# Kernel tuning notes

Hardware: AMD Instinct MI355X
Metric: run time of the kernel (lower is better)

Reference implementation:

```python
import jax, jax.numpy as jnp
import numpy as np


def setup_inputs() -> dict:
    key = jax.random.key(0)
    pred = jax.random.normal(key, (16, 4, 768, 768), dtype=jnp.float32)
    return {"pred": pred}


def _largest_cc(mask):
    """Largest 4-connected component of a 2D boolean mask, as float32 0/1.

    Equivalent to scipy.ndimage.label (default 4-connectivity) followed by
    keeping the largest label. Uses min-label flood propagation: each
    foreground pixel starts with its raster index; iterated neighbor-min
    converges so every pixel holds its component's minimum pixel index
    (the 'root'). Ties in size resolve to the smallest root, which matches
    scipy's label-order tie-breaking (labels assigned in raster order).
    """
    H, W = mask.shape
    HW = H * W
    idx = jnp.arange(HW, dtype=jnp.int32).reshape(H, W)
    BIG = jnp.int32(HW)  # sentinel for background
    lbl0 = jnp.where(mask, idx, BIG)

    def body(carry):
        lbl, _ = carry
        p = jnp.pad(lbl, 1, constant_values=HW)
        nb = jnp.minimum(jnp.minimum(p[:-2, 1:-1], p[2:, 1:-1]),
                         jnp.minimum(p[1:-1, :-2], p[1:-1, 2:]))
        new = jnp.where(mask, jnp.minimum(lbl, nb), BIG)
        return new, jnp.any(new != lbl)

    lbl, _ = jax.lax.while_loop(lambda c: c[1], body, (lbl0, jnp.any(mask)))

    # component sizes keyed by root pixel index; background bucket = HW
    sizes = jax.ops.segment_sum(mask.ravel().astype(jnp.int32), lbl.ravel(),
                                num_segments=HW + 1)
    sizes = sizes.at[HW].set(0)
    root = jnp.argmax(sizes).astype(jnp.int32)
    return ((lbl == root) & mask).astype(jnp.float32)


def reference(pred):
    B, C, H, W = pred.shape
    labels = jnp.argmax(pred, axis=1)  # [B, H, W]
    cls = jnp.arange(1, C, dtype=labels.dtype)
    masks = labels[:, None, :, :] == cls[None, :, None, None]  # [B, C-1, H, W]
    comp = jax.vmap(_largest_cc)(masks.reshape(-1, H, W)).reshape(B, C - 1, H, W)
    bg = 1.0 - jnp.clip(comp.sum(axis=1), 0.0, 1.0)  # channel 0
    return jnp.concatenate([bg[:, None], comp], axis=1)
```

## Files before the change

kernel.cpp:

```cpp
#include <hip/hip_runtime.h>
#include <stdint.h>

#define BB 16
#define CC 4
#define HH 768
#define WW 768
#define HW (HH * WW)
#define NPIX (BB * HW)
#define NIMG (BB * (CC - 1))
#define BEST_STRIDE 16

#define TS 64
#define TPI (WW / TS)
#define TILES_PER_IMG (TPI * TPI)
#define TPIX (TS * TS)
#define CCL_TPB 256

typedef unsigned long long ull;


__device__ __forceinline__ int find_root(int* P, int i) {
    int p = P[i];
    while (p != i) {
        int gp = P[p];
        P[i] = gp;
        i = p;
        p = gp;
    }
    return i;
}

__device__ __forceinline__ void merge(int* P, int a, int b) {
    a = find_root(P, a);
    b = find_root(P, b);
    while (a != b) {
        if (a < b) { int t = a; a = b; b = t; }
        int old = atomicCAS(&P[a], a, b);
        if (old == a) return;
        a = find_root(P, old);
        b = find_root(P, b);
    }
}


__device__ __forceinline__ int lfind(int* P, int i) {
    int p = P[i];
    while (p != i) {
        int gp = P[p];
        P[i] = gp;
        i = p;
        p = gp;
    }
    return i;
}

__device__ __forceinline__ void lmerge(int* P, int a, int b) {
    a = lfind(P, a);
    b = lfind(P, b);
    while (a != b) {
        if (a < b) { int t = a; a = b; b = t; }
        int old = atomicCAS(&P[a], a, b);
        if (old == a) return;
        a = lfind(P, old);
        b = lfind(P, b);
    }
}

__device__ __forceinline__ ull umax64(ull a, ull b) { return a > b ? a : b; }


__global__ __launch_bounds__(CCL_TPB) void k_tile_ccl(
        const float* __restrict__ pred,
        uint8_t* __restrict__ labels,
        int* __restrict__ parent,
        uint32_t* __restrict__ counts,
        ull* __restrict__ best) {
    __shared__ __align__(16) int sp[TPIX];
    __shared__ __align__(16) uint8_t slab[TPIX];
    __shared__ int changed;

    if (blockIdx.x == 0) {
        for (int i = threadIdx.x; i < NIMG * BEST_STRIDE; i += CCL_TPB) best[i] = 0ull;
    }

    const int tid = (int)threadIdx.x;
    const int img = blockIdx.x / TILES_PER_IMG;
    const int tile = blockIdx.x % TILES_PER_IMG;
    const int tr = (tile / TPI) * TS;
    const int tc = (tile % TPI) * TS;
    const float* pb = pred + (size_t)img * CC * HW;
    const int imgbase = img * HW;

    for (int k = 0; k < TPIX; k += CCL_TPB * 4) {
        int li = k + tid * 4;
        int gi = (tr + (li >> 6)) * WW + tc + (li & 63);
        float4 v0 = *(const float4*)&pb[gi];
        float4 v1 = *(const float4*)&pb[gi + HW];
        float4 v2 = *(const float4*)&pb[gi + 2 * HW];
        float4 v3 = *(const float4*)&pb[gi + 3 * HW];
        const float* a0 = &v0.x; const float* a1 = &v1.x;
        const float* a2 = &v2.x; const float* a3 = &v3.x;
        uchar4 lout;
        uint8_t* lj = &lout.x;
        #pragma unroll
        for (int j = 0; j < 4; ++j) {
            int lab = 0;
            float bv = a0[j];
            if (a1[j] > bv) { bv = a1[j]; lab = 1; }
            if (a2[j] > bv) { bv = a2[j]; lab = 2; }
            if (a3[j] > bv) { bv = a3[j]; lab = 3; }
            lj[j] = (uint8_t)lab;
        }
        *(uchar4*)&slab[li] = lout;
        *(uchar4*)&labels[imgbase + gi] = lout;
    }
    __syncthreads();

    const int c = tid & 63;

    #pragma unroll 1
    for (int it = 0; it < TPIX / CCL_TPB; ++it) {
        int li = it * CCL_TPB + tid;
        int lab = slab[li];
        int labL = __shfl_up(lab, 1, 64);
        bool isStart = lab && (c == 0 || labL != lab);
        ull mask = __ballot(isStart);
        int v = li;
        if (lab) {
            ull mle = mask & (~0ull >> (63 - c));
            v = (li & ~63) + (63 - __clzll(mle));
        }
        sp[li] = v;
    }
    __syncthreads();

    #pragma unroll 1
    for (int it = 0; it < TPIX / CCL_TPB; ++it) {
        int li = it * CCL_TPB + tid;
        int lab = slab[li];
        int labU = (li >= TS) ? (int)slab[li - TS] : 0;
        int labL = __shfl_up(lab, 1, 64);
        int labUL = __shfl_up(labU, 1, 64);
        if (lab && labU == lab) {
            if (c == 0 || !(labL == lab && labUL == lab))
                lmerge(sp, li, li - TS);
        }
    }
    __syncthreads();

    for (;;) {
        if (tid == 0) changed = 0;
        __syncthreads();
        int any = 0;
        #pragma unroll 1
        for (int it = 0; it < TPIX / CCL_TPB; ++it) {
            int li = it * CCL_TPB + tid;
            int v = sp[li];
            int w = sp[v];
            if (w != v) { sp[li] = w; any = 1; }
        }
        if (any) changed = 1;
        __syncthreads();
        int go = changed;
        __syncthreads();
        if (!go) break;
    }

    #pragma unroll 1
    for (int it = 0; it < TPIX / CCL_TPB; ++it) {
        int li = it * CCL_TPB + tid;
        int lab = slab[li];
        int labL = __shfl_up(lab, 1, 64);
        bool isStart = lab && (c == 0 || labL != lab);
        bool isEnd = lab && (c == 63 || (int)slab[li + 1] != lab);
        ull endmask = __ballot(isEnd);
        if (isStart) {
            ull mge = endmask & (~0ull << c);
            int epos = __ffsll((long long)mge) - 1;
            int runlen = epos - c + 1;
            int root = sp[li] & 0xFFFF;
            atomicAdd((unsigned int*)&sp[root], (unsigned int)runlen << 16);
        }
    }
    __syncthreads();

    for (int k = 0; k < TPIX; k += CCL_TPB * 4) {
        int li = k + tid * 4;
        int gi = imgbase + (tr + (li >> 6)) * WW + tc + (li & 63);
        uchar4 lv = *(const uchar4*)&slab[li];
        int4 sv = *(const int4*)&sp[li];
        const uint8_t* lj = &lv.x;
        const int* sj = &sv.x;
        int4 pout; uint4 cout;
        int* pj = &pout.x; uint32_t* cj = &cout.x;
        #pragma unroll
        for (int j = 0; j < 4; ++j) {
            int root = sj[j] & 0xFFFF;
            if (lj[j]) {
                pj[j] = imgbase + (tr + (root >> 6)) * WW + tc + (root & 63);
                cj[j] = (root == li + j) ? ((uint32_t)sj[j] >> 16) : 0u;
            } else {
                pj[j] = -1;
                cj[j] = 0u;
            }
        }
        *(int4*)&parent[gi] = pout;
        *(uint4*)&counts[gi] = cout;
    }
}

#define VEDGES ((TPI - 1) * HH)
#define EDGES_PER_IMG (2 * (TPI - 1) * HH)
__global__ void k_border_merge(const uint8_t* __restrict__ labels, int* parent) {
    int t = blockIdx.x * blockDim.x + threadIdx.x;
    if (t >= BB * EDGES_PER_IMG) return;
    int img = t / EDGES_PER_IMG;
    int e = t % EDGES_PER_IMG;
    int a, b;
    if (e < VEDGES) {
        int j = e / HH, r = e % HH;
        int c = j * TS + TS - 1;
        a = r * WW + c;
        b = a + 1;
    } else {
        e -= VEDGES;
        int j = e / WW, c = e % WW;
        int r = j * TS + TS - 1;
        a = r * WW + c;
        b = a + WW;
    }
    int ga = img * HW + a, gb = img * HW + b;
    uint8_t la = labels[ga];
    if (la && labels[gb] == la) merge(parent, ga, gb);
}

__global__ void k_compress(int* __restrict__ parent, uint32_t* __restrict__ counts) {
    int t = blockIdx.x * blockDim.x + threadIdx.x;
    if (t >= NPIX) return;
    uint32_t cnt = counts[t];
    if (!cnt) return;
    int g = parent[t];
    if (g == t) return;
    while (true) { int pg = parent[g]; if (pg == g) break; g = pg; }
    parent[t] = g;
    atomicAdd(&counts[g], cnt);
    counts[t] = 0;
}

#define BEST_BLK_PER_IMG 144
#define BEST_TPB 256
#define BEST_PIX_PER_BLK (HW / BEST_BLK_PER_IMG)
__global__ void k_best(const uint8_t* __restrict__ labels,
                       const uint32_t* __restrict__ counts,
                       ull* __restrict__ best) {
    __shared__ ull sw[(BEST_TPB / 64) * 3];
    int img = blockIdx.x / BEST_BLK_PER_IMG;
    int chunk = blockIdx.x % BEST_BLK_PER_IMG;
    int base = img * HW + chunk * BEST_PIX_PER_BLK;

    ull l0 = 0, l1 = 0, l2 = 0;
    for (int k = 0; k < BEST_PIX_PER_BLK; k += BEST_TPB * 4) {
        int t = base + k + (int)threadIdx.x * 4;
        uint4 cv = *(const uint4*)&counts[t];
        if (cv.x | cv.y | cv.z | cv.w) {
            uchar4 lv = *(const uchar4*)&labels[t];
            uint32_t cs[4] = {cv.x, cv.y, cv.z, cv.w};
            uint8_t ls[4] = {lv.x, lv.y, lv.z, lv.w};
            #pragma unroll
            for (int j = 0; j < 4; ++j) {
                if (cs[j]) {
                    int cc = (int)ls[j] - 1;
                    ull key = ((ull)cs[j] << 32) | (ull)(~(uint32_t)(t + j));
                    if (cc == 0) l0 = umax64(l0, key);
                    else if (cc == 1) l1 = umax64(l1, key);
                    else l2 = umax64(l2, key);
                }
            }
        }
    }
    #pragma unroll
    for (int m = 1; m < 64; m <<= 1) {
        l0 = umax64(l0, __shfl_xor(l0, m, 64));
        l1 = umax64(l1, __shfl_xor(l1, m, 64));
        l2 = umax64(l2, __shfl_xor(l2, m, 64));
    }
    int lane = threadIdx.x & 63;
    int wid = threadIdx.x >> 6;
    if (lane == 0) { sw[wid * 3 + 0] = l0; sw[wid * 3 + 1] = l1; sw[wid * 3 + 2] = l2; }
    __syncthreads();
    if (threadIdx.x < 3) {
        ull m = 0;
        for (int w = 0; w < BEST_TPB / 64; ++w) m = umax64(m, sw[w * 3 + threadIdx.x]);
        if (m) atomicMax(&best[(img * 3 + (int)threadIdx.x) * BEST_STRIDE], m);
    }
}

__global__ void k_output(const uint8_t* __restrict__ labels,
                         const int* __restrict__ parent,
                         const ull* __restrict__ best,
                         float* __restrict__ out) {
    int q = blockIdx.x * blockDim.x + threadIdx.x;
    if (q >= NPIX / 4) return;
    int t = q * 4;
    int b = t / HW;
    int i = t - b * HW;
    uchar4 lv = *(const uchar4*)&labels[t];
    int4 pv = *(const int4*)&parent[t];
    int root[3];
    root[0] = (int)(~(uint32_t)best[(b * 3 + 0) * BEST_STRIDE]);
    root[1] = (int)(~(uint32_t)best[(b * 3 + 1) * BEST_STRIDE]);
    root[2] = (int)(~(uint32_t)best[(b * 3 + 2) * BEST_STRIDE]);

    uint8_t ls[4] = {lv.x, lv.y, lv.z, lv.w};
    int ps[4] = {pv.x, pv.y, pv.z, pv.w};
    float fg[4];
    #pragma unroll
    for (int j = 0; j < 4; ++j) {
        int g = -1;
        if (ps[j] >= 0) g = parent[ps[j]];
        fg[j] = (ls[j] && g == root[ls[j] - 1]) ? 1.0f : 0.0f;
    }

    float4 o0, o1, o2, o3;
    float* c0 = &o0.x; float* c1 = &o1.x; float* c2 = &o2.x; float* c3 = &o3.x;
    #pragma unroll
    for (int j = 0; j < 4; ++j) {
        c0[j] = 1.0f - fg[j];
        c1[j] = (ls[j] == 1) ? fg[j] : 0.0f;
        c2[j] = (ls[j] == 2) ? fg[j] : 0.0f;
        c3[j] = (ls[j] == 3) ? fg[j] : 0.0f;
    }
    float* o = out + (size_t)b * CC * HW + i;
    *(float4*)&o[0] = o0;
    *(float4*)&o[HW] = o1;
    *(float4*)&o[2 * HW] = o2;
    *(float4*)&o[3 * HW] = o3;
}


extern "C" void kernel_launch(void* const* d_in, const int* in_sizes, int n_in,
                              void* d_out, int out_size, void* d_ws, size_t ws_size,
                              hipStream_t stream) {
    const float* pred = (const float*)d_in[0];
    float* out = (float*)d_out;

    uint8_t* labels = (uint8_t*)d_ws;
    int* parent = (int*)((char*)d_ws + NPIX);
    ull* best = (ull*)((char*)d_ws + NPIX + (size_t)NPIX * 4);
    uint32_t* counts = (uint32_t*)d_out;

    const int TPB = 256;

    k_tile_ccl<<<BB * TILES_PER_IMG, CCL_TPB, 0, stream>>>(pred, labels, parent, counts, best);
    k_border_merge<<<(BB * EDGES_PER_IMG + TPB - 1) / TPB, TPB, 0, stream>>>(labels, parent);
    k_compress<<<(NPIX + TPB - 1) / TPB, TPB, 0, stream>>>(parent, counts);
    k_best<<<BB * BEST_BLK_PER_IMG, BEST_TPB, 0, stream>>>(labels, counts, best);
    k_output<<<(NPIX / 4 + TPB - 1) / TPB, TPB, 0, stream>>>(labels, parent, best, out);
}
```

Before: 155.3 us.

## Split argmax into separate kernel and replace iterative pointer jumping with direct root chase

```diff
diff --git a/kernel.cpp b/kernel.cpp
--- a/kernel.cpp
+++ b/kernel.cpp
@@ -69,50 +69,54 @@
 __device__ __forceinline__ ull umax64(ull a, ull b) { return a > b ? a : b; }
 
 
-__global__ __launch_bounds__(CCL_TPB) void k_tile_ccl(
-        const float* __restrict__ pred,
-        uint8_t* __restrict__ labels,
+__global__ void k_argmax(const float* __restrict__ pred,
+                         uint8_t* __restrict__ labels,
+                         ull* __restrict__ best) {
+    int q = blockIdx.x * blockDim.x + threadIdx.x;
+    if (q < NIMG * BEST_STRIDE) best[q] = 0ull;
+    if (q >= NPIX / 4) return;
+    int t = q * 4;
+    int b = t / HW;
+    int i = t - b * HW;
+    const float* p = pred + (size_t)b * CC * HW + i;
+    float4 v0 = *(const float4*)&p[0];
+    float4 v1 = *(const float4*)&p[HW];
+    float4 v2 = *(const float4*)&p[2 * HW];
+    float4 v3 = *(const float4*)&p[3 * HW];
+    const float* a0 = &v0.x; const float* a1 = &v1.x;
+    const float* a2 = &v2.x; const float* a3 = &v3.x;
+    uchar4 lout;
+    uint8_t* lj = &lout.x;
+    #pragma unroll
+    for (int j = 0; j < 4; ++j) {
+        int lab = 0;
+        float bv = a0[j];
+        if (a1[j] > bv) { bv = a1[j]; lab = 1; }
+        if (a2[j] > bv) { bv = a2[j]; lab = 2; }
+        if (a3[j] > bv) { bv = a3[j]; lab = 3; }
+        lj[j] = (uint8_t)lab;
+    }
+    *(uchar4*)&labels[t] = lout;
+}
+
+__global__ __launch_bounds__(CCL_TPB) void k_ccl(
+        const uint8_t* __restrict__ labels,
         int* __restrict__ parent,
-        uint32_t* __restrict__ counts,
-        ull* __restrict__ best) {
+        uint32_t* __restrict__ counts) {
     __shared__ __align__(16) int sp[TPIX];
     __shared__ __align__(16) uint8_t slab[TPIX];
-    __shared__ int changed;
-
-    if (blockIdx.x == 0) {
-        for (int i = threadIdx.x; i < NIMG * BEST_STRIDE; i += CCL_TPB) best[i] = 0ull;
-    }
 
     const int tid = (int)threadIdx.x;
     const int img = blockIdx.x / TILES_PER_IMG;
     const int tile = blockIdx.x % TILES_PER_IMG;
     const int tr = (tile / TPI) * TS;
     const int tc = (tile % TPI) * TS;
-    const float* pb = pred + (size_t)img * CC * HW;
     const int imgbase = img * HW;
 
     for (int k = 0; k < TPIX; k += CCL_TPB * 4) {
         int li = k + tid * 4;
-        int gi = (tr + (li >> 6)) * WW + tc + (li & 63);
-        float4 v0 = *(const float4*)&pb[gi];
-        float4 v1 = *(const float4*)&pb[gi + HW];
-        float4 v2 = *(const float4*)&pb[gi + 2 * HW];
-        float4 v3 = *(const float4*)&pb[gi + 3 * HW];
-        const float* a0 = &v0.x; const float* a1 = &v1.x;
-        const float* a2 = &v2.x; const float* a3 = &v3.x;
-        uchar4 lout;
-        uint8_t* lj = &lout.x;
-        #pragma unroll
-        for (int j = 0; j < 4; ++j) {
-            int lab = 0;
-            float bv = a0[j];
-            if (a1[j] > bv) { bv = a1[j]; lab = 1; }
-            if (a2[j] > bv) { bv = a2[j]; lab = 2; }
-            if (a3[j] > bv) { bv = a3[j]; lab = 3; }
-            lj[j] = (uint8_t)lab;
-        }
-        *(uchar4*)&slab[li] = lout;
-        *(uchar4*)&labels[imgbase + gi] = lout;
+        int gi = imgbase + (tr + (li >> 6)) * WW + tc + (li & 63);
+        *(uchar4*)&slab[li] = *(const uchar4*)&labels[gi];
     }
     __syncthreads();
 
@@ -148,23 +152,16 @@
     }
     __syncthreads();
 
-    for (;;) {
-        if (tid == 0) changed = 0;
-        __syncthreads();
-        int any = 0;
-        #pragma unroll 1
-        for (int it = 0; it < TPIX / CCL_TPB; ++it) {
-            int li = it * CCL_TPB + tid;
-            int v = sp[li];
-            int w = sp[v];
-            if (w != v) { sp[li] = w; any = 1; }
-        }
-        if (any) changed = 1;
-        __syncthreads();
-        int go = changed;
-        __syncthreads();
-        if (!go) break;
-    }
+    #pragma unroll 1
+    for (int it = 0; it < TPIX / CCL_TPB; ++it) {
+        int li = it * CCL_TPB + tid;
+        if (slab[li]) {
+            int p = sp[li];
+            while (true) { int pp = sp[p]; if (pp == p) break; p = pp; }
+            sp[li] = p;
+        }
+    }
+    __syncthreads();
 
     #pragma unroll 1
     for (int it = 0; it < TPIX / CCL_TPB; ++it) {
@@ -351,7 +348,8 @@
 
     const int TPB = 256;
 
-    k_tile_ccl<<<BB * TILES_PER_IMG, CCL_TPB, 0, stream>>>(pred, labels, parent, counts, best);
+    k_argmax<<<(NPIX / 4 + TPB - 1) / TPB, TPB, 0, stream>>>(pred, labels, best);
+    k_ccl<<<BB * TILES_PER_IMG, CCL_TPB, 0, stream>>>(labels, parent, counts);
     k_border_merge<<<(BB * EDGES_PER_IMG + TPB - 1) / TPB, TPB, 0, stream>>>(labels, parent);
     k_compress<<<(NPIX + TPB - 1) / TPB, TPB, 0, stream>>>(parent, counts);
     k_best<<<BB * BEST_BLK_PER_IMG, BEST_TPB, 0, stream>>>(labels, counts, best);
```

Result: slower. 171.5 us (+10.4%).
